# Performance work log

Hardware: AMD Instinct MI355X
Metric: run time of the kernel (lower is better)

The kernel has to match this reference:

```python
import jax, jax.numpy as jnp
import numpy as np

T, B_SZ = 1024, 1024
NX, NU, ND, NM, NDT, NH = 128, 64, 32, 32, 32, 128


def setup_inputs() -> dict:
    key = jax.random.key(0)
    ks = jax.random.split(key, 10)
    return {
        "x": jax.random.normal(ks[0], (B_SZ, NX), jnp.float32),
        "M_flow": jax.random.normal(ks[1], (T, B_SZ, NM), jnp.float32),
        "DT": jax.random.normal(ks[2], (T, B_SZ, NDT), jnp.float32),
        "D": jax.random.normal(ks[3], (T, B_SZ, ND), jnp.float32),
        # ConstrainedLinear(nx, nx): weight and scalar init with torch.rand -> uniform[0,1)
        "A_weight": jax.random.uniform(ks[4], (NX, NX), jnp.float32),
        "A_scalar": jax.random.uniform(ks[5], (NX, NX), jnp.float32),
        # nn.Linear(in, out, bias=False) weights are [out, in]
        "B_w": jax.random.normal(ks[6], (NX, NU), jnp.float32) * (1.0 / np.sqrt(NU)),
        "E_w": jax.random.normal(ks[7], (NX, ND), jnp.float32) * (1.0 / np.sqrt(ND)),
        "hf1_w": jax.random.normal(ks[8], (NH, NM + NDT), jnp.float32) * (1.0 / np.sqrt(NM + NDT)),
        "hf2_w": jax.random.normal(ks[9], (NU, NH), jnp.float32) * (1.0 / np.sqrt(NH)),
    }


def reference(x, M_flow, DT, D, A_weight, A_scalar, B_w, E_w, hf1_w, hf2_w):
    # Constrained weight: ((1 - 0.1*sigmoid(scalar)) * softmax(weight, dim=1)).T
    # It is constant across time, so compute once (torch redundantly recomputes it per step).
    s_clamped = 1.0 - 0.1 * jax.nn.sigmoid(A_scalar)
    W_eff = (s_clamped * jax.nn.softmax(A_weight, axis=1)).T  # [nx, nx]

    # Per-step control input u_t depends only on exogenous M_flow/DT -> vectorize over time.
    md = jnp.concatenate([M_flow, DT], axis=2)                # [T, B, n_m+n_dT]
    h = jax.nn.relu(jnp.einsum('tbi,hi->tbh', md, hf1_w))     # [T, B, n_hidden]
    u = jax.nn.relu(jnp.einsum('tbh,uh->tbu', h, hf2_w))      # [T, B, nu]

    # Precompute additive drive B(u_t) + E(d_t); only x@W_eff is sequential.
    drive = jnp.einsum('tbu,xu->tbx', u, B_w) + jnp.einsum('tbd,xd->tbx', D, E_w)

    def step(x_prev, drive_t):
        x_new = x_prev @ W_eff + drive_t
        return x_new, x_new

    _, X = jax.lax.scan(step, x, drive)  # X: [T, B, nx]
    Y = X[:, :, -1]                      # [T, B]
    return X, Y
```

## Files before the change

kernel.cpp:

```cpp
#include <hip/hip_runtime.h>

typedef _Float16 h4 __attribute__((ext_vector_type(4)));
typedef _Float16 h8 __attribute__((ext_vector_type(8)));
typedef float f4 __attribute__((ext_vector_type(4)));

#define MFMA16(a, b, c) __builtin_amdgcn_mfma_f32_16x16x32_f16((a), (b), (c), 0, 0, 0)

static constexpr int TT  = 1024;
static constexpr int BS  = 1024;
static constexpr int LCH = 32;
static constexpr int NCH = 32;
static constexpr size_t XTOT = (size_t)TT * BS * 128;

static constexpr size_t WS_WT16 = 0;
static constexpr size_t WS_HF1  = 32768;
static constexpr size_t WS_HF2  = 49152;
static constexpr size_t WS_BW   = 65536;
static constexpr size_t WS_EW   = 81920;
static constexpr size_t WS_W32  = 90112;
static constexpr size_t WS_F    = 131072;
static constexpr size_t WS_INIT = WS_F + (size_t)NCH * BS * 128 * 4;

template <typename T>
__device__ inline T ntload(const T* p) { return __builtin_nontemporal_load(p); }

__global__ void prep_kernel(const float* __restrict__ Aw, const float* __restrict__ As,
                            const float* __restrict__ hf1, const float* __restrict__ hf2,
                            const float* __restrict__ Bw, const float* __restrict__ Ew,
                            char* __restrict__ ws)
{
    const int tid = threadIdx.x;
    const int bid = blockIdx.x;
    if (bid < 128) {
        __shared__ float red[128];
        const int n = bid;
        const float a = Aw[n * 128 + tid];
        red[tid] = a;
        __syncthreads();
        for (int s = 64; s > 0; s >>= 1) {
            if (tid < s) red[tid] = fmaxf(red[tid], red[tid + s]);
            __syncthreads();
        }
        const float mx = red[0];
        __syncthreads();
        const float e = expf(a - mx);
        red[tid] = e;
        __syncthreads();
        for (int s = 64; s > 0; s >>= 1) {
            if (tid < s) red[tid] += red[tid + s];
            __syncthreads();
        }
        const float sm  = e / red[0];
        const float asv = As[n * 128 + tid];
        const float sc  = 1.0f - 0.1f * (1.0f / (1.0f + expf(-asv)));
        ((_Float16*)(ws + WS_WT16))[n * 128 + tid] = (_Float16)(sc * sm);
    } else {
        const int b2 = bid - 128;
        for (int i = b2 * 128 + tid; i < 8192; i += 32 * 128) {
            ((_Float16*)(ws + WS_HF1))[i] = (_Float16)hf1[i];
            ((_Float16*)(ws + WS_HF2))[i] = (_Float16)hf2[i];
            ((_Float16*)(ws + WS_BW))[i]  = (_Float16)Bw[i];
            if (i < 4096) ((_Float16*)(ws + WS_EW))[i] = (_Float16)Ew[i];
        }
    }
}

__global__ void w32_kernel(char* __restrict__ ws)
{
    const int tid  = threadIdx.x;
    const int lane = tid & 63;
    const int w    = tid >> 6;
    const int cl   = lane & 15;
    const int gq   = lane >> 4;
    constexpr int LDP = 136;

    __shared__ __align__(16) _Float16 G[2][128 * LDP];
    __shared__ __align__(16) _Float16 H[2][128 * LDP];

    const _Float16* Wt16 = (const _Float16*)(ws + WS_WT16);
    for (int i = tid; i < 2048; i += 256)
        *(h8*)&G[0][(i >> 4) * LDP + (i & 15) * 8] = *(const h8*)&Wt16[i * 8];
    __syncthreads();
    for (int i = tid; i < 16384; i += 256) {
        const int r = i >> 7, cc = i & 127;
        H[0][cc * LDP + r] = G[0][r * LDP + cc];
    }
    __syncthreads();

    int cur = 0;
    for (int s = 0; s < 5; ++s) {
        const _Float16* Gs = G[cur];
        const _Float16* Hs = H[cur];
        _Float16* Gd = G[cur ^ 1];
        _Float16* Hd = H[cur ^ 1];
        f4 aG[8][2], aH[8][2];
#pragma unroll
        for (int mt = 0; mt < 8; ++mt)
#pragma unroll
            for (int nt = 0; nt < 2; ++nt) { aG[mt][nt] = f4{}; aH[mt][nt] = f4{}; }
#pragma unroll
        for (int kk = 0; kk < 4; ++kk) {
            h8 bG0 = *(const h8*)&Hs[((w * 2 + 0) * 16 + cl) * LDP + kk * 32 + gq * 8];
            h8 bG1 = *(const h8*)&Hs[((w * 2 + 1) * 16 + cl) * LDP + kk * 32 + gq * 8];
            h8 bH0 = *(const h8*)&Gs[((w * 2 + 0) * 16 + cl) * LDP + kk * 32 + gq * 8];
            h8 bH1 = *(const h8*)&Gs[((w * 2 + 1) * 16 + cl) * LDP + kk * 32 + gq * 8];
#pragma unroll
            for (int mt = 0; mt < 8; ++mt) {
                h8 ag = *(const h8*)&Gs[(mt * 16 + cl) * LDP + kk * 32 + gq * 8];
                h8 ah = *(const h8*)&Hs[(mt * 16 + cl) * LDP + kk * 32 + gq * 8];
                aG[mt][0] = MFMA16(ag, bG0, aG[mt][0]);
                aG[mt][1] = MFMA16(ag, bG1, aG[mt][1]);
                aH[mt][0] = MFMA16(ah, bH0, aH[mt][0]);
                aH[mt][1] = MFMA16(ah, bH1, aH[mt][1]);
            }
        }
#pragma unroll
        for (int mt = 0; mt < 8; ++mt)
#pragma unroll
            for (int nt = 0; nt < 2; ++nt) {
                h4 hg, hh;
#pragma unroll
                for (int r = 0; r < 4; ++r) {
                    hg[r] = (_Float16)aG[mt][nt][r];
                    hh[r] = (_Float16)aH[mt][nt][r];
                }
                const int col  = (w * 2 + nt) * 16 + cl;
                const int rowb = mt * 16 + gq * 4;
                *(h4*)&Hd[col * LDP + rowb] = hg;
                *(h4*)&Gd[col * LDP + rowb] = hh;
            }
        __syncthreads();
        cur ^= 1;
    }
    _Float16* W32 = (_Float16*)(ws + WS_W32);
    for (int i = tid; i < 2048; i += 256)
        *(h8*)&W32[i * 8] = *(const h8*)&G[cur][(i >> 4) * LDP + (i & 15) * 8];
}

template <bool FINAL>
__global__ __launch_bounds__(256, 2)
void fused_scan(const float* __restrict__ Mfl, const float* __restrict__ DTi,
                const float* __restrict__ Din, char* __restrict__ ws,
                float* __restrict__ Xout, float* __restrict__ Yout)
{
    const int tid  = threadIdx.x;
    const int lane = tid & 63;
    const int w    = tid >> 6;
    const int cl   = lane & 15;
    const int gq   = lane >> 4;
    const int bt   = blockIdx.x & 63;
    const int c    = blockIdx.x >> 6;
    const int b0   = bt * 16;

    const _Float16* Hf1  = (const _Float16*)(ws + WS_HF1);
    const _Float16* Hf2  = (const _Float16*)(ws + WS_HF2);
    const _Float16* Bw16 = (const _Float16*)(ws + WS_BW);
    const _Float16* Ew16 = (const _Float16*)(ws + WS_EW);
    const _Float16* Wt16 = (const _Float16*)(ws + WS_WT16);
    float* Fbuf          = (float*)(ws + WS_F);
    const float* Init    = (const float*)(ws + WS_INIT);

    __shared__ __align__(16) _Float16 mds[4][16 * 64];
    __shared__ __align__(16) _Float16 dts[4][16 * 32];
    __shared__ __align__(16) _Float16 hs[4][16 * 128];
    __shared__ __align__(16) _Float16 us[4][16 * 64];
    __shared__ __align__(16) _Float16 xsh[2][16 * 128];

    h8 hf1f[2][2], bwf[2][2], ewf[2], hf2f[4];
#pragma unroll
    for (int nt = 0; nt < 2; ++nt) {
        const int ng = w * 32 + nt * 16 + cl;
#pragma unroll
        for (int kk = 0; kk < 2; ++kk) {
            hf1f[nt][kk] = *(const h8*)&Hf1[ng * 64 + kk * 32 + gq * 8];
            bwf[nt][kk]  = *(const h8*)&Bw16[ng * 64 + kk * 32 + gq * 8];
        }
        ewf[nt] = *(const h8*)&Ew16[ng * 32 + gq * 8];
    }
    {
        const int ng = w * 16 + cl;
#pragma unroll
        for (int kk = 0; kk < 4; ++kk)
            hf2f[kk] = *(const h8*)&Hf2[ng * 128 + kk * 32 + gq * 8];
    }
    h8 wfp[2][4];
#pragma unroll
    for (int nt = 0; nt < 2; ++nt)
#pragma unroll
        for (int kt = 0; kt < 4; ++kt)
            wfp[nt][kt] =
                *(const h8*)&Wt16[(w * 32 + nt * 16 + cl) * 128 + kt * 32 + gq * 8];

    if constexpr (FINAL) {
        const int row = tid >> 4, c8 = tid & 15;
        const float* src = &Init[((size_t)c * BS + b0 + row) * 128 + c8 * 8];
        f4 v0 = *(const f4*)src, v1 = *(const f4*)(src + 4);
        h8 hv;
#pragma unroll
        for (int j = 0; j < 4; ++j) { hv[j] = (_Float16)v0[j]; hv[4 + j] = (_Float16)v1[j]; }
        *(h8*)&xsh[0][row * 128 + ((c8 ^ row) & 15) * 8] = hv;
    } else {
        h8 z = {};
        *(h8*)&xsh[0][tid * 8] = z;
    }

    const int qrow = (tid & 127) >> 3;
    const int qc4  = (tid & 7) * 4;
    f4 pm[4], pd[4];
    auto GLOAD = [&](int g) {
#pragma unroll
        for (int s = 0; s < 4; ++s) {
            const size_t t  = (size_t)c * LCH + g * 4 + s;
            const size_t rb = (t * BS + b0 + qrow) * 32 + qc4;
            pm[s] = (tid < 128) ? ntload((const f4*)&Mfl[rb]) : ntload((const f4*)&DTi[rb]);
            if (tid < 128) pd[s] = ntload((const f4*)&Din[rb]);
        }
    };
    GLOAD(0);

    _Float16* xcur = xsh[0];
    _Float16* xnxt = xsh[1];

    for (int g = 0; g < 8; ++g) {
#pragma unroll
        for (int s = 0; s < 4; ++s) {
            const int col = (tid < 128) ? qc4 : (32 + qc4);
            h4 hv;
#pragma unroll
            for (int j = 0; j < 4; ++j) hv[j] = (_Float16)pm[s][j];
            *(h4*)&mds[s][qrow * 64 + (((col >> 3) ^ (qrow & 7)) * 8) + (col & 7)] = hv;
            if (tid < 128) {
                h4 h2;
#pragma unroll
                for (int j = 0; j < 4; ++j) h2[j] = (_Float16)pd[s][j];
                *(h4*)&dts[s][qrow * 32 + (((qc4 >> 3) ^ (qrow & 3)) * 8) + (qc4 & 7)] = h2;
            }
        }
        if (g < 7) GLOAD(g + 1);
        __syncthreads();

#pragma unroll
        for (int s = 0; s < 4; ++s) {
            f4 ha0 = {}, ha1 = {};
#pragma unroll
            for (int kk = 0; kk < 2; ++kk) {
                h8 a = *(const h8*)&mds[s][cl * 64 + (((kk * 4 + gq) ^ (cl & 7)) * 8)];
                ha0 = MFMA16(hf1f[0][kk], a, ha0);
                ha1 = MFMA16(hf1f[1][kk], a, ha1);
            }
#pragma unroll
            for (int nt = 0; nt < 2; ++nt) {
                const int nb8 = w * 4 + nt * 2 + (gq >> 1);
                h4 hv;
#pragma unroll
                for (int r = 0; r < 4; ++r)
                    hv[r] = (_Float16)fmaxf(nt ? ha1[r] : ha0[r], 0.f);
                *(h4*)&hs[s][cl * 128 + ((nb8 ^ cl) & 15) * 8 + (gq & 1) * 4] = hv;
            }
        }
        __syncthreads();

#pragma unroll
        for (int s = 0; s < 4; ++s) {
            f4 ua = {};
#pragma unroll
            for (int kt = 0; kt < 4; ++kt) {
                h8 a = *(const h8*)&hs[s][cl * 128 + (((kt * 4 + gq) ^ cl) & 15) * 8];
                ua = MFMA16(hf2f[kt], a, ua);
            }
            const int ub8 = w * 2 + (gq >> 1);
            h4 uv;
#pragma unroll
            for (int r = 0; r < 4; ++r) uv[r] = (_Float16)fmaxf(ua[r], 0.f);
            *(h4*)&us[s][cl * 64 + ((ub8 ^ (cl & 7)) & 7) * 8 + (gq & 1) * 4] = uv;
        }
        __syncthreads();

        h4 dv[4][2];
#pragma unroll
        for (int s = 0; s < 4; ++s) {
            f4 a20 = {}, a21 = {};
#pragma unroll
            for (int kk = 0; kk < 2; ++kk) {
                h8 a = *(const h8*)&us[s][cl * 64 + (((kk * 4 + gq) ^ (cl & 7)) & 7) * 8];
                a20 = MFMA16(bwf[0][kk], a, a20);
                a21 = MFMA16(bwf[1][kk], a, a21);
            }
            {
                h8 ad = *(const h8*)&dts[s][cl * 32 + ((gq ^ (cl & 3)) * 8)];
                a20 = MFMA16(ewf[0], ad, a20);
                a21 = MFMA16(ewf[1], ad, a21);
            }
#pragma unroll
            for (int r = 0; r < 4; ++r) {
                dv[s][0][r] = (_Float16)a20[r];
                dv[s][1][r] = (_Float16)a21[r];
            }
        }

#pragma unroll
        for (int s = 0; s < 4; ++s) {
            h8 xf[4];
#pragma unroll
            for (int kt = 0; kt < 4; ++kt)
                xf[kt] = *(const h8*)&xcur[cl * 128 + (((kt * 4 + gq) ^ cl) & 15) * 8];
            f4 acc0, acc1;
#pragma unroll
            for (int r = 0; r < 4; ++r) {
                acc0[r] = (float)dv[s][0][r];
                acc1[r] = (float)dv[s][1][r];
            }
#pragma unroll
            for (int kt = 0; kt < 4; ++kt) {
                acc0 = MFMA16(wfp[0][kt], xf[kt], acc0);
                acc1 = MFMA16(wfp[1][kt], xf[kt], acc1);
            }

            if constexpr (FINAL) {
                const size_t t = (size_t)c * LCH + g * 4 + s;
                float* xp = &Xout[(t * BS + b0 + cl) * 128 + w * 32 + gq * 4];
                __builtin_nontemporal_store(acc0, (f4*)xp);
                __builtin_nontemporal_store(acc1, (f4*)(xp + 16));
                if (w == 3 && gq == 3)
                    __builtin_nontemporal_store(acc1[3], &Yout[t * BS + b0 + cl]);
            }
            const bool last = (g == 7) && (s == 3);
            if (!FINAL && last) {
                float* fp = &Fbuf[((size_t)c * BS + b0 + cl) * 128 + w * 32 + gq * 4];
                *(f4*)fp = acc0;
                *(f4*)(fp + 16) = acc1;
            }
            if (!last) {
#pragma unroll
                for (int nt = 0; nt < 2; ++nt) {
                    h4 hv;
#pragma unroll
                    for (int r = 0; r < 4; ++r) hv[r] = (_Float16)(nt ? acc1[r] : acc0[r]);
                    const int nb8 = w * 4 + nt * 2 + (gq >> 1);
                    *(h4*)&xnxt[cl * 128 + ((nb8 ^ cl) & 15) * 8 + (gq & 1) * 4] = hv;
                }
                __syncthreads();
                _Float16* tmp = xcur; xcur = xnxt; xnxt = tmp;
            }
        }
    }
}

__global__ __launch_bounds__(64, 1)
void carry_kernel(const float* __restrict__ x0, char* __restrict__ ws,
                  int cc_lo, int n_steps, int copy0)
{
    const int lane = threadIdx.x;
    const int cl = lane & 15, gq = lane >> 4;
    const int b0 = blockIdx.x * 16;

    const _Float16* W32 = (const _Float16*)(ws + WS_W32);
    const float* Fbuf   = (const float*)(ws + WS_F);
    float* Init         = (float*)(ws + WS_INIT);

    __shared__ __align__(16) _Float16 tbuf[16 * 128];

    h8 wf[8][4];
#pragma unroll
    for (int nt = 0; nt < 8; ++nt)
#pragma unroll
        for (int kt = 0; kt < 4; ++kt)
            wf[nt][kt] = *(const h8*)&W32[(nt * 16 + cl) * 128 + kt * 32 + gq * 8];

    h8 xf[4];
    {
        f4 iv[8];
#pragma unroll
        for (int nt = 0; nt < 8; ++nt)
            iv[nt] = *(const f4*)&x0[(size_t)(b0 + cl) * 128 + nt * 16 + gq * 4];
        if (copy0) {
#pragma unroll
            for (int nt = 0; nt < 8; ++nt)
                *(f4*)&Init[((size_t)cc_lo * BS + b0 + cl) * 128 + nt * 16 + gq * 4] = iv[nt];
        }
#pragma unroll
        for (int nt = 0; nt < 8; ++nt) {
            h4 hv;
#pragma unroll
            for (int r = 0; r < 4; ++r) hv[r] = (_Float16)iv[nt][r];
            *(h4*)&tbuf[cl * 128 + (((nt * 2 + (gq >> 1)) ^ cl) & 15) * 8 + (gq & 1) * 4] = hv;
        }
#pragma unroll
        for (int kt = 0; kt < 4; ++kt)
            xf[kt] = *(const h8*)&tbuf[cl * 128 + (((kt * 4 + gq) ^ cl) & 15) * 8];
    }

    for (int i = 1; i <= n_steps; ++i) {
        const int cc = cc_lo + i;
        f4 acc[8];
#pragma unroll
        for (int nt = 0; nt < 8; ++nt)
            acc[nt] = *(const f4*)&Fbuf[((size_t)(cc - 1) * BS + b0 + cl) * 128 + nt * 16 + gq * 4];
#pragma unroll
        for (int kt = 0; kt < 4; ++kt)
#pragma unroll
            for (int nt = 0; nt < 8; ++nt)
                acc[nt] = MFMA16(wf[nt][kt], xf[kt], acc[nt]);
#pragma unroll
        for (int nt = 0; nt < 8; ++nt)
            *(f4*)&Init[((size_t)cc * BS + b0 + cl) * 128 + nt * 16 + gq * 4] = acc[nt];
        if (i < n_steps) {
#pragma unroll
            for (int nt = 0; nt < 8; ++nt) {
                h4 hv;
#pragma unroll
                for (int r = 0; r < 4; ++r) hv[r] = (_Float16)acc[nt][r];
                *(h4*)&tbuf[cl * 128 + (((nt * 2 + (gq >> 1)) ^ cl) & 15) * 8 + (gq & 1) * 4] = hv;
            }
#pragma unroll
            for (int kt = 0; kt < 4; ++kt)
                xf[kt] = *(const h8*)&tbuf[cl * 128 + (((kt * 4 + gq) ^ cl) & 15) * 8];
        }
    }
}

extern "C" void kernel_launch(void* const* d_in, const int* in_sizes, int n_in,
                              void* d_out, int out_size, void* d_ws, size_t ws_size,
                              hipStream_t stream)
{
    const float* x_in = (const float*)d_in[0];
    const float* Mfl  = (const float*)d_in[1];
    const float* DTi  = (const float*)d_in[2];
    const float* Din  = (const float*)d_in[3];
    const float* Aw   = (const float*)d_in[4];
    const float* As   = (const float*)d_in[5];
    const float* Bw   = (const float*)d_in[6];
    const float* Ew   = (const float*)d_in[7];
    const float* hf1  = (const float*)d_in[8];
    const float* hf2  = (const float*)d_in[9];
    char* ws    = (char*)d_ws;
    float* Xout = (float*)d_out;
    float* Yout = Xout + XTOT;

    prep_kernel<<<dim3(160), dim3(128), 0, stream>>>(Aw, As, hf1, hf2, Bw, Ew, ws);
    w32_kernel<<<dim3(1), dim3(256), 0, stream>>>(ws);

    fused_scan<false><<<dim3(31 * 64), dim3(256), 0, stream>>>(Mfl, DTi, Din, ws,
                                                               nullptr, nullptr);
    carry_kernel<<<dim3(64), dim3(64), 0, stream>>>(x_in, ws, 0, 31, 1);
    fused_scan<true><<<dim3(32 * 64), dim3(256), 0, stream>>>(Mfl, DTi, Din, ws,
                                                              Xout, Yout);
}
```

Before: 422.8 us.

## Load MFMA input fragments directly from global, dropping LDS staging and a barrier

Each lane now loads M_flow, DT and D straight from global memory in the MFMA B-operand layout and packs them to fp16 in registers. This removes the mds/dts shared-memory staging, its swizzled stores and one __syncthreads per group. The prefetch of the next group moves after the drive MFMAs, and the drive accumulators stay in fp32 rather than round-tripping through fp16. Packed RTZ conversion (cvt_pkrtz) replaces the per-element casts, and carry_kernel's unused parameters are simplified. The trade-offs are that every wave re-reads the inputs (more redundant global traffic), register pressure rises, and round-toward-zero conversion slightly changes numerics.

```diff
diff --git a/kernel.cpp b/kernel.cpp
--- a/kernel.cpp
+++ b/kernel.cpp
@@ -1,7 +1,9 @@
 #include <hip/hip_runtime.h>
 
+typedef _Float16 h2 __attribute__((ext_vector_type(2)));
 typedef _Float16 h4 __attribute__((ext_vector_type(4)));
 typedef _Float16 h8 __attribute__((ext_vector_type(8)));
+typedef __fp16 g2 __attribute__((ext_vector_type(2)));
 typedef float f4 __attribute__((ext_vector_type(4)));
 
 #define MFMA16(a, b, c) __builtin_amdgcn_mfma_f32_16x16x32_f16((a), (b), (c), 0, 0, 0)
@@ -23,6 +25,33 @@
 
 template <typename T>
 __device__ inline T ntload(const T* p) { return __builtin_nontemporal_load(p); }
+
+__device__ inline h4 pk4(f4 a) {
+    g2 p0 = __builtin_amdgcn_cvt_pkrtz(a[0], a[1]);
+    g2 p1 = __builtin_amdgcn_cvt_pkrtz(a[2], a[3]);
+    h4 r;
+    r[0] = (_Float16)p0[0]; r[1] = (_Float16)p0[1];
+    r[2] = (_Float16)p1[0]; r[3] = (_Float16)p1[1];
+    return r;
+}
+__device__ inline h8 pk8(f4 a, f4 b) {
+    g2 p0 = __builtin_amdgcn_cvt_pkrtz(a[0], a[1]);
+    g2 p1 = __builtin_amdgcn_cvt_pkrtz(a[2], a[3]);
+    g2 p2 = __builtin_amdgcn_cvt_pkrtz(b[0], b[1]);
+    g2 p3 = __builtin_amdgcn_cvt_pkrtz(b[2], b[3]);
+    h8 r;
+    r[0] = (_Float16)p0[0]; r[1] = (_Float16)p0[1];
+    r[2] = (_Float16)p1[0]; r[3] = (_Float16)p1[1];
+    r[4] = (_Float16)p2[0]; r[5] = (_Float16)p2[1];
+    r[6] = (_Float16)p3[0]; r[7] = (_Float16)p3[1];
+    return r;
+}
+__device__ inline f4 relu4(f4 a) {
+    f4 r;
+#pragma unroll
+    for (int j = 0; j < 4; ++j) r[j] = fmaxf(a[j], 0.f);
+    return r;
+}
 
 __global__ void prep_kernel(const float* __restrict__ Aw, const float* __restrict__ As,
                             const float* __restrict__ hf1, const float* __restrict__ hf2,
@@ -160,8 +189,6 @@
     float* Fbuf          = (float*)(ws + WS_F);
     const float* Init    = (const float*)(ws + WS_INIT);
 
-    __shared__ __align__(16) _Float16 mds[4][16 * 64];
-    __shared__ __align__(16) _Float16 dts[4][16 * 32];
     __shared__ __align__(16) _Float16 hs[4][16 * 128];
     __shared__ __align__(16) _Float16 us[4][16 * 64];
     __shared__ __align__(16) _Float16 xsh[2][16 * 128];
@@ -204,57 +231,41 @@
         *(h8*)&xsh[0][tid * 8] = z;
     }
 
-    const int qrow = (tid & 127) >> 3;
-    const int qc4  = (tid & 7) * 4;
-    f4 pm[4], pd[4];
+    h8 fm[4], fdt[4], fd[4];
     auto GLOAD = [&](int g) {
 #pragma unroll
         for (int s = 0; s < 4; ++s) {
             const size_t t  = (size_t)c * LCH + g * 4 + s;
-            const size_t rb = (t * BS + b0 + qrow) * 32 + qc4;
-            pm[s] = (tid < 128) ? ntload((const f4*)&Mfl[rb]) : ntload((const f4*)&DTi[rb]);
-            if (tid < 128) pd[s] = ntload((const f4*)&Din[rb]);
+            const size_t ba = (t * BS + b0 + cl) * 32 + gq * 8;
+            f4 a0 = ntload((const f4*)&Mfl[ba]);
+            f4 a1 = ntload((const f4*)&Mfl[ba + 4]);
+            f4 b0v = ntload((const f4*)&DTi[ba]);
+            f4 b1v = ntload((const f4*)&DTi[ba + 4]);
+            f4 d0 = ntload((const f4*)&Din[ba]);
+            f4 d1 = ntload((const f4*)&Din[ba + 4]);
+            fm[s]  = pk8(a0, a1);
+            fdt[s] = pk8(b0v, b1v);
+            fd[s]  = pk8(d0, d1);
         }
     };
     GLOAD(0);
 
     _Float16* xcur = xsh[0];
     _Float16* xnxt = xsh[1];
+    __syncthreads();
 
     for (int g = 0; g < 8; ++g) {
-#pragma unroll
-        for (int s = 0; s < 4; ++s) {
-            const int col = (tid < 128) ? qc4 : (32 + qc4);
-            h4 hv;
-#pragma unroll
-            for (int j = 0; j < 4; ++j) hv[j] = (_Float16)pm[s][j];
-            *(h4*)&mds[s][qrow * 64 + (((col >> 3) ^ (qrow & 7)) * 8) + (col & 7)] = hv;
-            if (tid < 128) {
-                h4 h2;
-#pragma unroll
-                for (int j = 0; j < 4; ++j) h2[j] = (_Float16)pd[s][j];
-                *(h4*)&dts[s][qrow * 32 + (((qc4 >> 3) ^ (qrow & 3)) * 8) + (qc4 & 7)] = h2;
-            }
-        }
-        if (g < 7) GLOAD(g + 1);
-        __syncthreads();
-
 #pragma unroll
         for (int s = 0; s < 4; ++s) {
             f4 ha0 = {}, ha1 = {};
-#pragma unroll
-            for (int kk = 0; kk < 2; ++kk) {
-                h8 a = *(const h8*)&mds[s][cl * 64 + (((kk * 4 + gq) ^ (cl & 7)) * 8)];
-                ha0 = MFMA16(hf1f[0][kk], a, ha0);
-                ha1 = MFMA16(hf1f[1][kk], a, ha1);
-            }
+            ha0 = MFMA16(hf1f[0][0], fm[s], ha0);
+            ha1 = MFMA16(hf1f[1][0], fm[s], ha1);
+            ha0 = MFMA16(hf1f[0][1], fdt[s], ha0);
+            ha1 = MFMA16(hf1f[1][1], fdt[s], ha1);
 #pragma unroll
             for (int nt = 0; nt < 2; ++nt) {
                 const int nb8 = w * 4 + nt * 2 + (gq >> 1);
-                h4 hv;
-#pragma unroll
-                for (int r = 0; r < 4; ++r)
-                    hv[r] = (_Float16)fmaxf(nt ? ha1[r] : ha0[r], 0.f);
+                h4 hv = pk4(relu4(nt ? ha1 : ha0));
                 *(h4*)&hs[s][cl * 128 + ((nb8 ^ cl) & 15) * 8 + (gq & 1) * 4] = hv;
             }
         }
@@ -269,14 +280,12 @@
                 ua = MFMA16(hf2f[kt], a, ua);
             }
             const int ub8 = w * 2 + (gq >> 1);
-            h4 uv;
-#pragma unroll
-            for (int r = 0; r < 4; ++r) uv[r] = (_Float16)fmaxf(ua[r], 0.f);
+            h4 uv = pk4(relu4(ua));
             *(h4*)&us[s][cl * 64 + ((ub8 ^ (cl & 7)) & 7) * 8 + (gq & 1) * 4] = uv;
         }
         __syncthreads();
 
-        h4 dv[4][2];
+        f4 dv0[4], dv1[4];
 #pragma unroll
         for (int s = 0; s < 4; ++s) {
             f4 a20 = {}, a21 = {};
@@ -286,17 +295,13 @@
                 a20 = MFMA16(bwf[0][kk], a, a20);
                 a21 = MFMA16(bwf[1][kk], a, a21);
             }
-            {
-                h8 ad = *(const h8*)&dts[s][cl * 32 + ((gq ^ (cl & 3)) * 8)];
-                a20 = MFMA16(ewf[0], ad, a20);
-                a21 = MFMA16(ewf[1], ad, a21);
-            }
-#pragma unroll
-            for (int r = 0; r < 4; ++r) {
-                dv[s][0][r] = (_Float16)a20[r];
-                dv[s][1][r] = (_Float16)a21[r];
-            }
-        }
+            a20 = MFMA16(ewf[0], fd[s], a20);
+            a21 = MFMA16(ewf[1], fd[s], a21);
+            dv0[s] = a20;
+            dv1[s] = a21;
+        }
+
+        if (g < 7) GLOAD(g + 1);
 
 #pragma unroll
         for (int s = 0; s < 4; ++s) {
@@ -304,12 +309,7 @@
 #pragma unroll
             for (int kt = 0; kt < 4; ++kt)
                 xf[kt] = *(const h8*)&xcur[cl * 128 + (((kt * 4 + gq) ^ cl) & 15) * 8];
-            f4 acc0, acc1;
-#pragma unroll
-            for (int r = 0; r < 4; ++r) {
-                acc0[r] = (float)dv[s][0][r];
-                acc1[r] = (float)dv[s][1][r];
-            }
+            f4 acc0 = dv0[s], acc1 = dv1[s];
 #pragma unroll
             for (int kt = 0; kt < 4; ++kt) {
                 acc0 = MFMA16(wfp[0][kt], xf[kt], acc0);
@@ -347,8 +347,7 @@
 }
 
 __global__ __launch_bounds__(64, 1)
-void carry_kernel(const float* __restrict__ x0, char* __restrict__ ws,
-                  int cc_lo, int n_steps, int copy0)
+void carry_kernel(const float* __restrict__ x0, char* __restrict__ ws, int n_steps)
 {
     const int lane = threadIdx.x;
     const int cl = lane & 15, gq = lane >> 4;
@@ -373,11 +372,9 @@
 #pragma unroll
         for (int nt = 0; nt < 8; ++nt)
             iv[nt] = *(const f4*)&x0[(size_t)(b0 + cl) * 128 + nt * 16 + gq * 4];
-        if (copy0) {
-#pragma unroll
-            for (int nt = 0; nt < 8; ++nt)
-                *(f4*)&Init[((size_t)cc_lo * BS + b0 + cl) * 128 + nt * 16 + gq * 4] = iv[nt];
-        }
+#pragma unroll
+        for (int nt = 0; nt < 8; ++nt)
+            *(f4*)&Init[(size_t)(b0 + cl) * 128 + nt * 16 + gq * 4] = iv[nt];
 #pragma unroll
         for (int nt = 0; nt < 8; ++nt) {
             h4 hv;
@@ -390,8 +387,7 @@
             xf[kt] = *(const h8*)&tbuf[cl * 128 + (((kt * 4 + gq) ^ cl) & 15) * 8];
     }
 
-    for (int i = 1; i <= n_steps; ++i) {
-        const int cc = cc_lo + i;
+    for (int cc = 1; cc <= n_steps; ++cc) {
         f4 acc[8];
 #pragma unroll
         for (int nt = 0; nt < 8; ++nt)
@@ -404,7 +400,7 @@
 #pragma unroll
         for (int nt = 0; nt < 8; ++nt)
             *(f4*)&Init[((size_t)cc * BS + b0 + cl) * 128 + nt * 16 + gq * 4] = acc[nt];
-        if (i < n_steps) {
+        if (cc < n_steps) {
 #pragma unroll
             for (int nt = 0; nt < 8; ++nt) {
                 h4 hv;
@@ -442,7 +438,7 @@
 
     fused_scan<false><<<dim3(31 * 64), dim3(256), 0, stream>>>(Mfl, DTi, Din, ws,
                                                                nullptr, nullptr);
-    carry_kernel<<<dim3(64), dim3(64), 0, stream>>>(x_in, ws, 0, 31, 1);
+    carry_kernel<<<dim3(64), dim3(64), 0, stream>>>(x_in, ws, 31);
     fused_scan<true><<<dim3(32 * 64), dim3(256), 0, stream>>>(Mfl, DTi, Din, ws,
                                                               Xout, Yout);
 }
```

Result: slower. 793.9 us (+87.8%).
